# Kernel optimization log

Measured on AMD Instinct MI355X. Metric: run time of the kernel, lower is better.

## Reference

```python
import jax, jax.numpy as jnp
import numpy as np
from jax import lax

USER_NUM = 60000
ITEM_NUM = 40000
N_NODES = USER_NUM + ITEM_NUM
EMB = 64
NNZ = 3200000
N_LAYERS = 3
ALPHA = 0.1


def setup_inputs() -> dict:
    key = jax.random.key(0)
    k1, k2, k3, k4, k5 = jax.random.split(key, 5)
    rows = jax.random.randint(k1, (NNZ,), 0, N_NODES, dtype=jnp.int32)
    cols = jax.random.randint(k2, (NNZ,), 0, N_NODES, dtype=jnp.int32)
    # normalized adjacency values are small positives
    vals = jax.random.uniform(k3, (NNZ,), dtype=jnp.float32) * 0.05
    user_emb = jax.random.normal(k4, (USER_NUM, EMB), dtype=jnp.float32) * 0.1
    item_emb = jax.random.normal(k5, (ITEM_NUM, EMB), dtype=jnp.float32) * 0.1
    return {"rows": rows, "cols": cols, "vals": vals,
            "user_emb": user_emb, "item_emb": item_emb}


def reference(rows, cols, vals, user_emb, item_emb):
    # ego = cat(user, item); e_out starts at zeros (first forward call).
    ego = jnp.concatenate([user_emb, item_emb], axis=0)  # [N, d]
    e0 = jnp.zeros_like(ego)

    def step(e, _):
        # torch.sparse.mm(A, e.clone().detach()) -> SpMM with stop_gradient,
        # matching the original's detach of the propagated state.
        gathered = vals[:, None] * lax.stop_gradient(e)[cols]  # [nnz, d]
        msg = jax.ops.segment_sum(gathered, rows, num_segments=N_NODES)
        e_new = (1.0 - ALPHA) * msg + ego
        return e_new, None

    e_out, _ = lax.scan(step, e0, None, length=N_LAYERS)
    return e_out[:USER_NUM], e_out[USER_NUM:]
```

## Files before the change

kernel.cpp:

```cpp
#include <hip/hip_runtime.h>
#include <hip/hip_fp16.h>


#define USER_NUM 60000
#define ITEM_NUM 40000
#define N_NODES  100000
#define EMB      64
#define NNZ      3200000
#define OMA       0.9f
#define BR       128
#define NB       782
#define TILE     4096
#define CAPB     4480
#define EPT      9

typedef float f32x4 __attribute__((ext_vector_type(4)));

__global__ __launch_bounds__(512) void bucket_scatter(const int* __restrict__ rows,
                                                      const int* __restrict__ cols,
                                                      const float* __restrict__ vals,
                                                      const float* __restrict__ ue,
                                                      const float* __restrict__ ie,
                                                      __half* __restrict__ ego_h,
                                                      int* __restrict__ bcursor,
                                                      int2* __restrict__ ebuf) {
    __shared__ int bins[NB + 1];
    __shared__ int lcur[NB];
    __shared__ int wsum[8];
    __shared__ int2 stage[TILE];
    __shared__ unsigned short sbk[TILE];
    int t = threadIdx.x;
    int lane = t & 63, w = t >> 6;

    {
        const int total8 = N_NODES * EMB / 8;
        const size_t usz = (size_t)USER_NUM * EMB;
        int u0 = blockIdx.x * 1024;
#pragma unroll
        for (int q = 0; q < 2; ++q) {
            int u = u0 + t + 512 * q;
            if (u < total8) {
                size_t f0 = (size_t)u * 8;
                const float4* s4 = (f0 < usz) ? (const float4*)(ue + f0)
                                              : (const float4*)(ie + (f0 - usz));
                float4 x = s4[0], y = s4[1];
                union { float4 f4; __half2 h2[4]; } o;
                o.h2[0] = __floats2half2_rn(x.x, x.y);
                o.h2[1] = __floats2half2_rn(x.z, x.w);
                o.h2[2] = __floats2half2_rn(y.x, y.y);
                o.h2[3] = __floats2half2_rn(y.z, y.w);
                ((float4*)ego_h)[u] = o.f4;
            }
        }
    }

    for (int b = t; b <= NB; b += 512) bins[b] = 0;
    __syncthreads();

    int e0 = blockIdx.x * TILE;
    int mybk[8], mypk[8];
    float myv[8];
#pragma unroll
    for (int j = 0; j < 8; ++j) {
        int i = e0 + t + 512 * j;
        mybk[j] = -1;
        if (i < NNZ) {
            int r = __builtin_nontemporal_load(&rows[i]);
            int c = __builtin_nontemporal_load(&cols[i]);
            myv[j]  = __builtin_nontemporal_load(&vals[i]) * OMA;
            mybk[j] = r >> 7;
            mypk[j] = c | ((r & 127) << 17);
            atomicAdd(&bins[mybk[j]], 1);
        }
    }
    __syncthreads();

    int b0 = t * 2;
    int r0 = (b0     < NB) ? bins[b0]     : 0;
    int r1 = (b0 + 1 < NB) ? bins[b0 + 1] : 0;
    int s = r0 + r1;
    int incl = s;
#pragma unroll
    for (int off = 1; off < 64; off <<= 1) {
        int v = __shfl_up(incl, off, 64);
        if (lane >= off) incl += v;
    }
    if (lane == 63) wsum[w] = incl;
    __syncthreads();
    int prefix = 0;
#pragma unroll
    for (int i = 0; i < 8; ++i) if (i < w) prefix += wsum[i];
    int excl = prefix + incl - s;
    if (b0     < NB) { bins[b0]     = excl; lcur[b0]     = excl; excl += r0; }
    if (b0 + 1 < NB) { bins[b0 + 1] = excl; lcur[b0 + 1] = excl; }
    if (t == 511) bins[NB] = prefix + incl;
    __syncthreads();

#pragma unroll
    for (int j = 0; j < 8; ++j) {
        if (mybk[j] >= 0) {
            int p = atomicAdd(&lcur[mybk[j]], 1);
            stage[p] = make_int2(mypk[j], __float_as_int(myv[j]));
            sbk[p] = (unsigned short)mybk[j];
        }
    }
    __syncthreads();

    for (int b = t; b < NB; b += 512) {
        int st = bins[b], en = bins[b + 1];
        int c = en - st;
        if (c > 0) lcur[b] = b * CAPB + atomicAdd(&bcursor[b], c) - st;
    }
    __syncthreads();

    int total = bins[NB];
    for (int i = t; i < total; i += 512) {
        int bk = sbk[i];
        ebuf[(size_t)(lcur[bk] + i)] = stage[i];
    }
}

__global__ __launch_bounds__(512) void sort_spmm1(const int* __restrict__ bcursor,
                                                  int2* __restrict__ ebuf,
                                                  int* __restrict__ row_start,
                                                  int* __restrict__ row_end,
                                                  const __half* __restrict__ ego_h,
                                                  __half* __restrict__ e2h) {
    __shared__ int2 stage[CAPB];
    __shared__ int rhist[BR], rofs[BR], rcur[BR];
    int bk = blockIdx.x, t = threadIdx.x;
    int s = bk * CAPB;
    int cnt = min(bcursor[bk], CAPB);

    if (t < BR) rhist[t] = 0;
    __syncthreads();

    int2 ev[EPT]; int erow[EPT];
#pragma unroll
    for (int j = 0; j < EPT; ++j) {
        int i = t + 512 * j;
        erow[j] = -1;
        if (i < cnt) {
            ev[j] = ebuf[(size_t)(s + i)];
            erow[j] = (ev[j].x >> 17) & 127;
            atomicAdd(&rhist[erow[j]], 1);
        }
    }
    __syncthreads();
    if (t < 64) {
        int h0 = rhist[2 * t], h1 = rhist[2 * t + 1];
        int pair = h0 + h1;
        int incl = pair;
#pragma unroll
        for (int off = 1; off < 64; off <<= 1) {
            int v = __shfl_up(incl, off, 64);
            if (t >= off) incl += v;
        }
        int base = incl - pair;
        rofs[2 * t]     = base;      rcur[2 * t]     = base;
        rofs[2 * t + 1] = base + h0; rcur[2 * t + 1] = base + h0;
    }
    __syncthreads();
    if (t < BR) {
        int r = (bk << 7) + t;
        if (r < N_NODES) {
            row_start[r] = s + rofs[t];
            row_end[r]   = s + rofs[t] + rhist[t];
        }
    }
#pragma unroll
    for (int j = 0; j < EPT; ++j) {
        if (erow[j] >= 0) {
            int p = atomicAdd(&rcur[erow[j]], 1);
            stage[p] = ev[j];
        }
    }
    __syncthreads();
    for (int i = t; i < cnt; i += 512) ebuf[(size_t)(s + i)] = stage[i];

    int lane  = t & 15;
    int qbase = (t & 63) & ~15;
    int g = t >> 4;
    const float2* srcv = (const float2*)ego_h;
#pragma unroll
    for (int rr = 0; rr < 4; ++rr) {
        int rl = (g << 2) | rr;
        int r  = (bk << 7) + rl;
        if (r >= N_NODES) break;
        union { float2 f2; __half2 h2[2]; } ei;
        ei.f2 = srcv[(size_t)r * 16 + lane];
        float2 i0 = __half22float2(ei.h2[0]);
        float2 i1 = __half22float2(ei.h2[1]);
        float4 acc = make_float4(i0.x, i0.y, i1.x, i1.y);
        int ss = rofs[rl];
        int ee = ss + rhist[rl];
        for (int k = ss; k < ee; k += 16) {
            int idx = k + lane;
            int2 cv = (idx < ee) ? stage[idx] : make_int2(0, 0);
#pragma unroll
            for (int j = 0; j < 16; ++j) {
                int   cj = __shfl(cv.x, qbase + j, 64) & 0x1FFFF;
                float vj = __int_as_float(__shfl(cv.y, qbase + j, 64));
                union { float2 f2; __half2 h2[2]; } u;
                u.f2 = srcv[(size_t)cj * 16 + lane];
                float2 a = __half22float2(u.h2[0]);
                float2 b = __half22float2(u.h2[1]);
                acc.x += vj * a.x; acc.y += vj * a.y;
                acc.z += vj * b.x; acc.w += vj * b.y;
            }
        }
        union { float2 f2; __half2 h2[2]; } o;
        o.h2[0] = __floats2half2_rn(acc.x, acc.y);
        o.h2[1] = __floats2half2_rn(acc.z, acc.w);
        ((float2*)e2h)[(size_t)r * 16 + lane] = o.f2;
    }
}

__global__ __launch_bounds__(512) void spmm2(const int* __restrict__ bcursor,
                                             const int* __restrict__ row_start,
                                             const int* __restrict__ row_end,
                                             const int2* __restrict__ ebuf,
                                             const __half* __restrict__ src,
                                             const __half* __restrict__ ego_h,
                                             float* __restrict__ outb) {
    __shared__ int2 stage[CAPB];
    int bk = blockIdx.x, t = threadIdx.x;
    int s = bk * CAPB;
    int cnt = min(bcursor[bk], CAPB);

    const unsigned long long* eb8 = (const unsigned long long*)ebuf;
    unsigned long long* st8 = (unsigned long long*)stage;
    for (int i = t; i < cnt; i += 512)
        st8[i] = __builtin_nontemporal_load(&eb8[(size_t)(s + i)]);
    __syncthreads();

    int lane  = t & 15;
    int qbase = (t & 63) & ~15;
    int g = t >> 4;
    const float2* srcv = (const float2*)src;
    const float2* egov = (const float2*)ego_h;
#pragma unroll
    for (int rr = 0; rr < 4; ++rr) {
        int rl = (g << 2) | rr;
        int r  = (bk << 7) + rl;
        if (r >= N_NODES) break;
        union { float2 f2; __half2 h2[2]; } ei;
        ei.f2 = egov[(size_t)r * 16 + lane];
        float2 i0 = __half22float2(ei.h2[0]);
        float2 i1 = __half22float2(ei.h2[1]);
        float4 acc = make_float4(i0.x, i0.y, i1.x, i1.y);
        int ss = row_start[r] - s;
        int ee = row_end[r] - s;
        for (int k = ss; k < ee; k += 16) {
            int idx = k + lane;
            int2 cv = (idx < ee) ? stage[idx] : make_int2(0, 0);
#pragma unroll
            for (int j = 0; j < 16; ++j) {
                int   cj = __shfl(cv.x, qbase + j, 64) & 0x1FFFF;
                float vj = __int_as_float(__shfl(cv.y, qbase + j, 64));
                union { float2 f2; __half2 h2[2]; } u;
                u.f2 = srcv[(size_t)cj * 16 + lane];
                float2 a = __half22float2(u.h2[0]);
                float2 b = __half22float2(u.h2[1]);
                acc.x += vj * a.x; acc.y += vj * a.y;
                acc.z += vj * b.x; acc.w += vj * b.y;
            }
        }
        f32x4 av = { acc.x, acc.y, acc.z, acc.w };
        __builtin_nontemporal_store(av, &((f32x4*)outb)[(size_t)r * 16 + lane]);
    }
}

extern "C" void kernel_launch(void* const* d_in, const int* in_sizes, int n_in,
                              void* d_out, int out_size, void* d_ws, size_t ws_size,
                              hipStream_t stream) {
    const int*   rows = (const int*)d_in[0];
    const int*   cols = (const int*)d_in[1];
    const float* vals = (const float*)d_in[2];
    const float* ue   = (const float*)d_in[3];
    const float* ie   = (const float*)d_in[4];
    float* out = (float*)d_out;

    char* ws = (char*)d_ws;
    __half* ego_h    = (__half*)ws;
    __half* e2h      = (__half*)(ws + 12800000);
    int2*   ebuf     = (int2*)(ws + 25600000);
    int*    row_s    = (int*)(ws + 53626880);
    int*    row_e    = (int*)(ws + 54026880);
    int*    bcursor  = (int*)(ws + 54426880);

    hipMemsetAsync(bcursor, 0, NB * sizeof(int), stream);

    const int tiles = (NNZ + TILE - 1) / TILE;
    bucket_scatter<<<tiles, 512, 0, stream>>>(rows, cols, vals, ue, ie, ego_h,
                                              bcursor, ebuf);
    sort_spmm1<<<NB, 512, 0, stream>>>(bcursor, ebuf, row_s, row_e, ego_h, e2h);
    spmm2<<<NB, 512, 0, stream>>>(bcursor, row_s, row_e, ebuf, e2h, ego_h, out);
}
```

Baseline: 268.8 us.

## Fuse scatter, sort and both SpMM layers into one cooperative kernel

Merges the bucket scatter, per-bucket row sort with first SpMM, and the second SpMM into a single cooperative kernel separated by grid.sync(). Each block keeps its sorted edges and row offsets in shared memory across the layers, so the second layer no longer reloads ebuf or reads row_start/row_end from global memory, and two kernel launch gaps disappear. The scatter drops the per-edge bucket-id array and finds each edge's bucket by binary search over the bin offsets instead. In exchange it needs all 782 blocks co-resident, has higher LDS pressure from the union, pays grid-wide sync cost, and falls back to a three-kernel path when occupancy is too low.

```diff
diff --git a/kernel.cpp b/kernel.cpp
--- a/kernel.cpp
+++ b/kernel.cpp
@@ -1,4 +1,5 @@
 #include <hip/hip_runtime.h>
+#include <hip/hip_cooperative_groups.h>
 #include <hip/hip_fp16.h>
 
 
@@ -14,28 +15,41 @@
 #define CAPB     4480
 #define EPT      9
 
+namespace cg = cooperative_groups;
 typedef float f32x4 __attribute__((ext_vector_type(4)));
 
-__global__ __launch_bounds__(512) void bucket_scatter(const int* __restrict__ rows,
-                                                      const int* __restrict__ cols,
-                                                      const float* __restrict__ vals,
-                                                      const float* __restrict__ ue,
-                                                      const float* __restrict__ ie,
-                                                      __half* __restrict__ ego_h,
-                                                      int* __restrict__ bcursor,
-                                                      int2* __restrict__ ebuf) {
-    __shared__ int bins[NB + 1];
-    __shared__ int lcur[NB];
-    __shared__ int wsum[8];
-    __shared__ int2 stage[TILE];
-    __shared__ unsigned short sbk[TILE];
-    int t = threadIdx.x;
-    int lane = t & 63, w = t >> 6;
+union ShMem {
+    struct {
+        int bins[NB + 1];
+        int lcur[NB];
+        int wsum[8];
+        int2 stage[TILE];
+    } sc;
+    struct {
+        int2 stage[CAPB];
+        int rhist[BR], rofs[BR], rcur[BR];
+    } sp;
+};
+
+__global__ __launch_bounds__(512, 8) void fused(const int* __restrict__ rows,
+                                                const int* __restrict__ cols,
+                                                const float* __restrict__ vals,
+                                                const float* __restrict__ ue,
+                                                const float* __restrict__ ie,
+                                                __half* __restrict__ ego_h,
+                                                __half* __restrict__ e2h,
+                                                int* __restrict__ bcursor,
+                                                int2* __restrict__ ebuf,
+                                                float* __restrict__ outb) {
+    __shared__ ShMem sh;
+    cg::grid_group grid = cg::this_grid();
+    int bk = blockIdx.x, t = threadIdx.x;
+    int lane64 = t & 63, w = t >> 6;
 
     {
         const int total8 = N_NODES * EMB / 8;
         const size_t usz = (size_t)USER_NUM * EMB;
-        int u0 = blockIdx.x * 1024;
+        int u0 = bk * 1024;
 #pragma unroll
         for (int q = 0; q < 2; ++q) {
             int u = u0 + t + 512 * q;
@@ -54,9 +68,231 @@
         }
     }
 
+    for (int b = t; b <= NB; b += 512) sh.sc.bins[b] = 0;
+    __syncthreads();
+
+    int e0 = bk * TILE;
+    int mybk[8], mypk[8];
+    float myv[8];
+#pragma unroll
+    for (int j = 0; j < 8; ++j) {
+        int i = e0 + t + 512 * j;
+        mybk[j] = -1;
+        if (i < NNZ) {
+            int r = __builtin_nontemporal_load(&rows[i]);
+            int c = __builtin_nontemporal_load(&cols[i]);
+            myv[j]  = __builtin_nontemporal_load(&vals[i]) * OMA;
+            mybk[j] = r >> 7;
+            mypk[j] = c | ((r & 127) << 17);
+            atomicAdd(&sh.sc.bins[mybk[j]], 1);
+        }
+    }
+    __syncthreads();
+
+    {
+        int b0 = t * 2;
+        int r0 = (b0     < NB) ? sh.sc.bins[b0]     : 0;
+        int r1 = (b0 + 1 < NB) ? sh.sc.bins[b0 + 1] : 0;
+        int s2 = r0 + r1;
+        int incl = s2;
+#pragma unroll
+        for (int off = 1; off < 64; off <<= 1) {
+            int v = __shfl_up(incl, off, 64);
+            if (lane64 >= off) incl += v;
+        }
+        if (lane64 == 63) sh.sc.wsum[w] = incl;
+        __syncthreads();
+        int prefix = 0;
+#pragma unroll
+        for (int i = 0; i < 8; ++i) if (i < w) prefix += sh.sc.wsum[i];
+        int excl = prefix + incl - s2;
+        if (b0     < NB) { sh.sc.bins[b0]     = excl; sh.sc.lcur[b0]     = excl; excl += r0; }
+        if (b0 + 1 < NB) { sh.sc.bins[b0 + 1] = excl; sh.sc.lcur[b0 + 1] = excl; }
+        if (t == 511) sh.sc.bins[NB] = prefix + incl;
+    }
+    __syncthreads();
+
+#pragma unroll
+    for (int j = 0; j < 8; ++j) {
+        if (mybk[j] >= 0) {
+            int p = atomicAdd(&sh.sc.lcur[mybk[j]], 1);
+            sh.sc.stage[p] = make_int2(mypk[j], __float_as_int(myv[j]));
+        }
+    }
+    __syncthreads();
+
+    for (int b = t; b < NB; b += 512) {
+        int st = sh.sc.bins[b], en = sh.sc.bins[b + 1];
+        int c = en - st;
+        if (c > 0) sh.sc.lcur[b] = b * CAPB + atomicAdd(&bcursor[b], c) - st;
+    }
+    __syncthreads();
+
+    {
+        int total = sh.sc.bins[NB];
+        for (int i = t; i < total; i += 512) {
+            int lo = 0, hi = NB;
+            while (hi - lo > 1) {
+                int mid = (lo + hi) >> 1;
+                if (sh.sc.bins[mid] <= i) lo = mid; else hi = mid;
+            }
+            ebuf[(size_t)(sh.sc.lcur[lo] + i)] = sh.sc.stage[i];
+        }
+    }
+
+    grid.sync();
+
+    int s = bk * CAPB;
+    int cnt = min(bcursor[bk], CAPB);
+
+    if (t < BR) sh.sp.rhist[t] = 0;
+    __syncthreads();
+
+    int2 ev[EPT]; int erow[EPT];
+#pragma unroll
+    for (int j = 0; j < EPT; ++j) {
+        int i = t + 512 * j;
+        erow[j] = -1;
+        if (i < cnt) {
+            ev[j] = ebuf[(size_t)(s + i)];
+            erow[j] = (ev[j].x >> 17) & 127;
+            atomicAdd(&sh.sp.rhist[erow[j]], 1);
+        }
+    }
+    __syncthreads();
+    if (t < 64) {
+        int h0 = sh.sp.rhist[2 * t], h1 = sh.sp.rhist[2 * t + 1];
+        int pair = h0 + h1;
+        int incl = pair;
+#pragma unroll
+        for (int off = 1; off < 64; off <<= 1) {
+            int v = __shfl_up(incl, off, 64);
+            if (t >= off) incl += v;
+        }
+        int base = incl - pair;
+        sh.sp.rofs[2 * t]     = base;      sh.sp.rcur[2 * t]     = base;
+        sh.sp.rofs[2 * t + 1] = base + h0; sh.sp.rcur[2 * t + 1] = base + h0;
+    }
+    __syncthreads();
+#pragma unroll
+    for (int j = 0; j < EPT; ++j) {
+        if (erow[j] >= 0) {
+            int p = atomicAdd(&sh.sp.rcur[erow[j]], 1);
+            sh.sp.stage[p] = ev[j];
+        }
+    }
+    __syncthreads();
+
+    int lane  = t & 15;
+    int qbase = (t & 63) & ~15;
+    int g = t >> 4;
+    const float2* srcv = (const float2*)ego_h;
+#pragma unroll
+    for (int rr = 0; rr < 4; ++rr) {
+        int rl = (g << 2) | rr;
+        int r  = (bk << 7) + rl;
+        if (r >= N_NODES) break;
+        union { float2 f2; __half2 h2[2]; } ei;
+        ei.f2 = srcv[(size_t)r * 16 + lane];
+        float2 i0 = __half22float2(ei.h2[0]);
+        float2 i1 = __half22float2(ei.h2[1]);
+        float4 acc = make_float4(i0.x, i0.y, i1.x, i1.y);
+        int ss = sh.sp.rofs[rl];
+        int ee = ss + sh.sp.rhist[rl];
+        for (int k = ss; k < ee; k += 16) {
+            int idx = k + lane;
+            int2 cv = (idx < ee) ? sh.sp.stage[idx] : make_int2(0, 0);
+#pragma unroll
+            for (int j = 0; j < 16; ++j) {
+                int   cj = __shfl(cv.x, qbase + j, 64) & 0x1FFFF;
+                float vj = __int_as_float(__shfl(cv.y, qbase + j, 64));
+                union { float2 f2; __half2 h2[2]; } u;
+                u.f2 = srcv[(size_t)cj * 16 + lane];
+                float2 a = __half22float2(u.h2[0]);
+                float2 b = __half22float2(u.h2[1]);
+                acc.x += vj * a.x; acc.y += vj * a.y;
+                acc.z += vj * b.x; acc.w += vj * b.y;
+            }
+        }
+        union { float2 f2; __half2 h2[2]; } o;
+        o.h2[0] = __floats2half2_rn(acc.x, acc.y);
+        o.h2[1] = __floats2half2_rn(acc.z, acc.w);
+        ((float2*)e2h)[(size_t)r * 16 + lane] = o.f2;
+    }
+
+    grid.sync();
+
+    const float2* src2 = (const float2*)e2h;
+#pragma unroll
+    for (int rr = 0; rr < 4; ++rr) {
+        int rl = (g << 2) | rr;
+        int r  = (bk << 7) + rl;
+        if (r >= N_NODES) break;
+        union { float2 f2; __half2 h2[2]; } ei;
+        ei.f2 = srcv[(size_t)r * 16 + lane];
+        float2 i0 = __half22float2(ei.h2[0]);
+        float2 i1 = __half22float2(ei.h2[1]);
+        float4 acc = make_float4(i0.x, i0.y, i1.x, i1.y);
+        int ss = sh.sp.rofs[rl];
+        int ee = ss + sh.sp.rhist[rl];
+        for (int k = ss; k < ee; k += 16) {
+            int idx = k + lane;
+            int2 cv = (idx < ee) ? sh.sp.stage[idx] : make_int2(0, 0);
+#pragma unroll
+            for (int j = 0; j < 16; ++j) {
+                int   cj = __shfl(cv.x, qbase + j, 64) & 0x1FFFF;
+                float vj = __int_as_float(__shfl(cv.y, qbase + j, 64));
+                union { float2 f2; __half2 h2[2]; } u;
+                u.f2 = src2[(size_t)cj * 16 + lane];
+                float2 a = __half22float2(u.h2[0]);
+                float2 b = __half22float2(u.h2[1]);
+                acc.x += vj * a.x; acc.y += vj * a.y;
+                acc.z += vj * b.x; acc.w += vj * b.y;
+            }
+        }
+        f32x4 av = { acc.x, acc.y, acc.z, acc.w };
+        __builtin_nontemporal_store(av, &((f32x4*)outb)[(size_t)r * 16 + lane]);
+    }
+}
+
+__global__ __launch_bounds__(512) void scatter_fb(const int* __restrict__ rows,
+                                                  const int* __restrict__ cols,
+                                                  const float* __restrict__ vals,
+                                                  const float* __restrict__ ue,
+                                                  const float* __restrict__ ie,
+                                                  __half* __restrict__ ego_h,
+                                                  int* __restrict__ bcursor,
+                                                  int2* __restrict__ ebuf) {
+    __shared__ int bins[NB + 1];
+    __shared__ int lcur[NB];
+    __shared__ int wsum[8];
+    __shared__ int2 stage[TILE];
+    __shared__ unsigned short sbk[TILE];
+    int t = threadIdx.x;
+    int lane = t & 63, w = t >> 6;
+    {
+        const int total8 = N_NODES * EMB / 8;
+        const size_t usz = (size_t)USER_NUM * EMB;
+        int u0 = blockIdx.x * 1024;
+#pragma unroll
+        for (int q = 0; q < 2; ++q) {
+            int u = u0 + t + 512 * q;
+            if (u < total8) {
+                size_t f0 = (size_t)u * 8;
+                const float4* s4 = (f0 < usz) ? (const float4*)(ue + f0)
+                                              : (const float4*)(ie + (f0 - usz));
+                float4 x = s4[0], y = s4[1];
+                union { float4 f4; __half2 h2[4]; } o;
+                o.h2[0] = __floats2half2_rn(x.x, x.y);
+                o.h2[1] = __floats2half2_rn(x.z, x.w);
+                o.h2[2] = __floats2half2_rn(y.x, y.y);
+                o.h2[3] = __floats2half2_rn(y.z, y.w);
+                ((float4*)ego_h)[u] = o.f4;
+            }
+        }
+    }
     for (int b = t; b <= NB; b += 512) bins[b] = 0;
     __syncthreads();
-
     int e0 = blockIdx.x * TILE;
     int mybk[8], mypk[8];
     float myv[8];
@@ -74,7 +310,6 @@
         }
     }
     __syncthreads();
-
     int b0 = t * 2;
     int r0 = (b0     < NB) ? bins[b0]     : 0;
     int r1 = (b0 + 1 < NB) ? bins[b0 + 1] : 0;
@@ -95,7 +330,6 @@
     if (b0 + 1 < NB) { bins[b0 + 1] = excl; lcur[b0 + 1] = excl; }
     if (t == 511) bins[NB] = prefix + incl;
     __syncthreads();
-
 #pragma unroll
     for (int j = 0; j < 8; ++j) {
         if (mybk[j] >= 0) {
@@ -105,14 +339,12 @@
         }
     }
     __syncthreads();
-
     for (int b = t; b < NB; b += 512) {
         int st = bins[b], en = bins[b + 1];
         int c = en - st;
         if (c > 0) lcur[b] = b * CAPB + atomicAdd(&bcursor[b], c) - st;
     }
     __syncthreads();
-
     int total = bins[NB];
     for (int i = t; i < total; i += 512) {
         int bk = sbk[i];
@@ -120,21 +352,19 @@
     }
 }
 
-__global__ __launch_bounds__(512) void sort_spmm1(const int* __restrict__ bcursor,
-                                                  int2* __restrict__ ebuf,
-                                                  int* __restrict__ row_start,
-                                                  int* __restrict__ row_end,
-                                                  const __half* __restrict__ ego_h,
-                                                  __half* __restrict__ e2h) {
+__global__ __launch_bounds__(512) void sort_spmm1_fb(const int* __restrict__ bcursor,
+                                                     int2* __restrict__ ebuf,
+                                                     int* __restrict__ row_start,
+                                                     int* __restrict__ row_end,
+                                                     const __half* __restrict__ ego_h,
+                                                     __half* __restrict__ e2h) {
     __shared__ int2 stage[CAPB];
     __shared__ int rhist[BR], rofs[BR], rcur[BR];
     int bk = blockIdx.x, t = threadIdx.x;
     int s = bk * CAPB;
     int cnt = min(bcursor[bk], CAPB);
-
     if (t < BR) rhist[t] = 0;
     __syncthreads();
-
     int2 ev[EPT]; int erow[EPT];
 #pragma unroll
     for (int j = 0; j < EPT; ++j) {
@@ -216,59 +446,48 @@
     }
 }
 
-__global__ __launch_bounds__(512) void spmm2(const int* __restrict__ bcursor,
-                                             const int* __restrict__ row_start,
-                                             const int* __restrict__ row_end,
-                                             const int2* __restrict__ ebuf,
-                                             const __half* __restrict__ src,
-                                             const __half* __restrict__ ego_h,
-                                             float* __restrict__ outb) {
-    __shared__ int2 stage[CAPB];
-    int bk = blockIdx.x, t = threadIdx.x;
-    int s = bk * CAPB;
-    int cnt = min(bcursor[bk], CAPB);
-
-    const unsigned long long* eb8 = (const unsigned long long*)ebuf;
-    unsigned long long* st8 = (unsigned long long*)stage;
-    for (int i = t; i < cnt; i += 512)
-        st8[i] = __builtin_nontemporal_load(&eb8[(size_t)(s + i)]);
-    __syncthreads();
-
-    int lane  = t & 15;
-    int qbase = (t & 63) & ~15;
-    int g = t >> 4;
+__global__ __launch_bounds__(256) void spmm2_fb(const int* __restrict__ row_start,
+                                                const int* __restrict__ row_end,
+                                                const int2* __restrict__ colval,
+                                                const __half* __restrict__ src,
+                                                const __half* __restrict__ ego_h,
+                                                float* __restrict__ outb) {
+    int tid = blockIdx.x * 256 + threadIdx.x;
+    int r = tid >> 4;
+    if (r >= N_NODES) return;
+    int lane  = threadIdx.x & 15;
+    int qbase = (threadIdx.x & 63) & ~15;
     const float2* srcv = (const float2*)src;
     const float2* egov = (const float2*)ego_h;
-#pragma unroll
-    for (int rr = 0; rr < 4; ++rr) {
-        int rl = (g << 2) | rr;
-        int r  = (bk << 7) + rl;
-        if (r >= N_NODES) break;
-        union { float2 f2; __half2 h2[2]; } ei;
-        ei.f2 = egov[(size_t)r * 16 + lane];
-        float2 i0 = __half22float2(ei.h2[0]);
-        float2 i1 = __half22float2(ei.h2[1]);
-        float4 acc = make_float4(i0.x, i0.y, i1.x, i1.y);
-        int ss = row_start[r] - s;
-        int ee = row_end[r] - s;
-        for (int k = ss; k < ee; k += 16) {
-            int idx = k + lane;
-            int2 cv = (idx < ee) ? stage[idx] : make_int2(0, 0);
-#pragma unroll
-            for (int j = 0; j < 16; ++j) {
-                int   cj = __shfl(cv.x, qbase + j, 64) & 0x1FFFF;
-                float vj = __int_as_float(__shfl(cv.y, qbase + j, 64));
-                union { float2 f2; __half2 h2[2]; } u;
-                u.f2 = srcv[(size_t)cj * 16 + lane];
-                float2 a = __half22float2(u.h2[0]);
-                float2 b = __half22float2(u.h2[1]);
-                acc.x += vj * a.x; acc.y += vj * a.y;
-                acc.z += vj * b.x; acc.w += vj * b.y;
-            }
-        }
-        f32x4 av = { acc.x, acc.y, acc.z, acc.w };
-        __builtin_nontemporal_store(av, &((f32x4*)outb)[(size_t)r * 16 + lane]);
-    }
+    union { float2 f2; __half2 h2[2]; } ei;
+    ei.f2 = egov[(size_t)r * 16 + lane];
+    float2 i0 = __half22float2(ei.h2[0]);
+    float2 i1 = __half22float2(ei.h2[1]);
+    float4 acc = make_float4(i0.x, i0.y, i1.x, i1.y);
+    const unsigned long long* cv8 = (const unsigned long long*)colval;
+    int s = row_start[r], e = row_end[r];
+    unsigned long long cv = 0;
+    if (s + lane < e) cv = __builtin_nontemporal_load(&cv8[(size_t)(s + lane)]);
+    for (int k = s; k < e; k += 16) {
+        int idxn = k + 16 + lane;
+        unsigned long long nv = 0;
+        if (idxn < e) nv = __builtin_nontemporal_load(&cv8[(size_t)idxn]);
+        int cx = (int)(cv & 0xFFFFFFFFull), cy = (int)(cv >> 32);
+#pragma unroll
+        for (int j = 0; j < 16; ++j) {
+            int   cj = __shfl(cx, qbase + j, 64) & 0x1FFFF;
+            float vj = __int_as_float(__shfl(cy, qbase + j, 64));
+            union { float2 f2; __half2 h2[2]; } u;
+            u.f2 = srcv[(size_t)cj * 16 + lane];
+            float2 a = __half22float2(u.h2[0]);
+            float2 b = __half22float2(u.h2[1]);
+            acc.x += vj * a.x; acc.y += vj * a.y;
+            acc.z += vj * b.x; acc.w += vj * b.y;
+        }
+        cv = nv;
+    }
+    f32x4 av = { acc.x, acc.y, acc.z, acc.w };
+    __builtin_nontemporal_store(av, &((f32x4*)outb)[(size_t)r * 16 + lane]);
 }
 
 extern "C" void kernel_launch(void* const* d_in, const int* in_sizes, int n_in,
@@ -291,9 +510,26 @@
 
     hipMemsetAsync(bcursor, 0, NB * sizeof(int), stream);
 
-    const int tiles = (NNZ + TILE - 1) / TILE;
-    bucket_scatter<<<tiles, 512, 0, stream>>>(rows, cols, vals, ue, ie, ego_h,
-                                              bcursor, ebuf);
-    sort_spmm1<<<NB, 512, 0, stream>>>(bcursor, ebuf, row_s, row_e, ego_h, e2h);
-    spmm2<<<NB, 512, 0, stream>>>(bcursor, row_s, row_e, ebuf, e2h, ego_h, out);
+    static int coopOK = -1;
+    if (coopOK < 0) {
+        int nb = 0;
+        hipError_t err = hipOccupancyMaxActiveBlocksPerMultiprocessor(&nb, fused, 512, 0);
+        coopOK = (err == hipSuccess && nb * 256 >= NB) ? 1 : 0;
+    }
+
+    if (coopOK) {
+        void* args[] = { (void*)&rows, (void*)&cols, (void*)&vals, (void*)&ue,
+                         (void*)&ie, (void*)&ego_h, (void*)&e2h, (void*)&bcursor,
+                         (void*)&ebuf, (void*)&out };
+        hipLaunchCooperativeKernel(reinterpret_cast<void*>(fused), dim3(NB),
+                                   dim3(512), args, 0, stream);
+    } else {
+        scatter_fb<<<NB, 512, 0, stream>>>(rows, cols, vals, ue, ie, ego_h,
+                                           bcursor, ebuf);
+        sort_spmm1_fb<<<NB, 512, 0, stream>>>(bcursor, ebuf, row_s, row_e,
+                                              ego_h, e2h);
+        const int spmmBlocks = (N_NODES * 16 + 255) / 256;
+        spmm2_fb<<<spmmBlocks, 256, 0, stream>>>(row_s, row_e, ebuf, e2h,
+                                                 ego_h, out);
+    }
 }
```

Measured after the change: 264.3 us. No clear change (-1.6%).
